# Performance work log

Hardware: AMD Instinct MI355X
Metric: run time of the kernel (lower is better)

The kernel has to match this reference:

```python
import jax, jax.numpy as jnp
import numpy as np

EMBED_DIM = 1024
NUM_HEADS = 16
HEAD_DIM = EMBED_DIM // NUM_HEADS


def setup_inputs() -> dict:
    key = jax.random.key(0)
    k_h, k_q, k_k, k_v, k_o = jax.random.split(key, 5)
    scale = 1.0 / np.sqrt(EMBED_DIM)
    return {
        "h": jax.random.normal(k_h, (2, 2048, EMBED_DIM), dtype=jnp.float32),
        "W_q": jax.random.normal(k_q, (EMBED_DIM, EMBED_DIM), dtype=jnp.float32) * scale,
        "W_k": jax.random.normal(k_k, (EMBED_DIM, EMBED_DIM), dtype=jnp.float32) * scale,
        "W_v": jax.random.normal(k_v, (EMBED_DIM, EMBED_DIM), dtype=jnp.float32) * scale,
        "W_o": jax.random.normal(k_o, (EMBED_DIM, EMBED_DIM), dtype=jnp.float32) * scale,
    }


def reference(h, W_q, W_k, W_v, W_o):
    B, S, E = h.shape
    H, D = NUM_HEADS, HEAD_DIM
    # nn.Linear stores weight as [out, in]; y = x @ W.T
    q = (h @ W_q.T).reshape(B, S, H, D).transpose(0, 2, 1, 3)  # [B,H,S,D]
    k = (h @ W_k.T).reshape(B, S, H, D).transpose(0, 2, 1, 3)
    v = (h @ W_v.T).reshape(B, S, H, D).transpose(0, 2, 1, 3)
    scores = jnp.einsum("bhsd,bhtd->bhst", q, k) / np.sqrt(D)
    attn = jax.nn.softmax(scores, axis=-1)
    ctx = jnp.einsum("bhst,bhtd->bhsd", attn, v)  # [B,H,S,D]
    ctx = ctx.transpose(0, 2, 1, 3).reshape(B, S, E)
    return ctx @ W_o.T
```

## Files before the change

kernel.cpp:

```cpp
#include <hip/hip_runtime.h>

#define B_ 2
#define S_ 2048
#define E_ 1024
#define H_ 16
#define D_ 64
#define M_ (B_*S_)

typedef __attribute__((ext_vector_type(8))) short bf16x8;
typedef __attribute__((ext_vector_type(4))) float f32x4;
typedef __attribute__((ext_vector_type(8))) unsigned short u16x8;
typedef __attribute__((ext_vector_type(4))) unsigned short u16x4;

__device__ __forceinline__ unsigned short f2bf(float f) {
  union { float f; unsigned u; } a; a.f = f;
  unsigned u = a.u;
  return (unsigned short)((u + 0x7FFFu + ((u >> 16) & 1u)) >> 16);
}

__device__ __forceinline__ void gload_lds16(const void* g, void* l) {
  __builtin_amdgcn_global_load_lds(
      (const __attribute__((address_space(1))) void*)g,
      (__attribute__((address_space(3))) void*)l, 16, 0, 0);
}

__global__ __launch_bounds__(256) void cvt_bf16(const float* __restrict__ src,
                                                unsigned short* __restrict__ dst,
                                                int n4, float scale) {
  int i = blockIdx.x * blockDim.x + threadIdx.x;
  if (i < n4) {
    float4 v = ((const float4*)src)[i];
    u16x4 o;
    o[0] = f2bf(v.x * scale);
    o[1] = f2bf(v.y * scale);
    o[2] = f2bf(v.z * scale);
    o[3] = f2bf(v.w * scale);
    ((u16x4*)dst)[i] = o;
  }
}

template<int OUT_BF16>
__device__ __forceinline__ void gemm_body(const unsigned short* __restrict__ A,
                                          const unsigned short* __restrict__ W,
                                          void* __restrict__ Cv,
                                          int row0, int col0, int N, int K,
                                          unsigned short* As, unsigned short* Bs) {
  const int tid = threadIdx.x;
  const int lane = tid & 63, wave = tid >> 6;
  const int wr = wave >> 1, wc = wave & 1;
  const int lq = lane & 15, lg = lane >> 4;
  f32x4 acc[4][4] = {};

  for (int kt = 0; kt < K; kt += 32) {
#pragma unroll
    for (int i = 0; i < 2; ++i) {
      int t = tid + i * 256;
      int rr = t >> 2;
      int sch = (t & 3) ^ ((rr >> 1) & 3);
      gload_lds16(A + (size_t)(row0 + rr) * K + kt + sch * 8, &As[t * 8]);
      gload_lds16(W + (size_t)(col0 + rr) * K + kt + sch * 8, &Bs[t * 8]);
    }
    __syncthreads();
    bf16x8 af[4], bfr[4];
#pragma unroll
    for (int mi = 0; mi < 4; ++mi) {
      int row = wr * 64 + mi * 16 + lq;
      af[mi] = *(const bf16x8*)&As[row * 32 + (lg ^ ((row >> 1) & 3)) * 8];
    }
#pragma unroll
    for (int ni = 0; ni < 4; ++ni) {
      int row = wc * 64 + ni * 16 + lq;
      bfr[ni] = *(const bf16x8*)&Bs[row * 32 + (lg ^ ((row >> 1) & 3)) * 8];
    }
#pragma unroll
    for (int mi = 0; mi < 4; ++mi)
#pragma unroll
      for (int ni = 0; ni < 4; ++ni)
        acc[mi][ni] = __builtin_amdgcn_mfma_f32_16x16x32_bf16(af[mi], bfr[ni], acc[mi][ni], 0, 0, 0);
    __syncthreads();
  }

#pragma unroll
  for (int mi = 0; mi < 4; ++mi)
#pragma unroll
    for (int ni = 0; ni < 4; ++ni) {
      int row = row0 + wr * 64 + mi * 16 + lg * 4;
      int col = col0 + wc * 64 + ni * 16 + lq;
#pragma unroll
      for (int r = 0; r < 4; ++r) {
        float v = acc[mi][ni][r];
        if (OUT_BF16) ((unsigned short*)Cv)[(size_t)(row + r) * N + col] = f2bf(v);
        else          ((float*)Cv)[(size_t)(row + r) * N + col] = v;
      }
    }
}

__global__ __launch_bounds__(256) void gemm_qkv(const unsigned short* __restrict__ A,
                                                const unsigned short* __restrict__ Wq,
                                                const unsigned short* __restrict__ Wk,
                                                const unsigned short* __restrict__ Wv,
                                                unsigned short* __restrict__ Qb,
                                                unsigned short* __restrict__ Kb,
                                                unsigned short* __restrict__ Vb) {
  __shared__ unsigned short As[128 * 32];
  __shared__ unsigned short Bs[128 * 32];
  const int mat = blockIdx.y >> 3;
  const int col0 = (blockIdx.y & 7) * 128;
  const unsigned short* W = (mat == 0) ? Wq : (mat == 1) ? Wk : Wv;
  unsigned short* C = (mat == 0) ? Qb : (mat == 1) ? Kb : Vb;
  gemm_body<1>(A, W, C, blockIdx.x * 128, col0, E_, E_, As, Bs);
}

__global__ __launch_bounds__(256) void gemm_out(const unsigned short* __restrict__ A,
                                                const unsigned short* __restrict__ W,
                                                float* __restrict__ C) {
  __shared__ unsigned short As[128 * 32];
  __shared__ unsigned short Bs[128 * 32];
  gemm_body<0>(A, W, C, blockIdx.x * 128, blockIdx.y * 128, E_, E_, As, Bs);
}

__global__ __launch_bounds__(256) void transpose_v(const unsigned short* __restrict__ V,
                                                   unsigned short* __restrict__ VT) {
  __shared__ unsigned short tile[64][72];
  const int tid = threadIdx.x;
  const int s0 = blockIdx.x * 64;
  const int h = blockIdx.y;
  const int b = blockIdx.z;
  const int r = tid >> 3;
  const int c = (tid & 7) * 8;
  const unsigned short* src = V + ((size_t)(b * S_) + s0) * E_ + h * 64;
#pragma unroll
  for (int i = 0; i < 2; ++i) {
    int rr = r + i * 32;
    u16x8 v = *(const u16x8*)(src + (size_t)rr * E_ + c);
#pragma unroll
    for (int j = 0; j < 8; ++j) tile[rr][c + j] = v[j];
  }
  __syncthreads();
  unsigned short* dst = VT + ((size_t)((b * H_ + h) * 64)) * S_ + s0;
#pragma unroll
  for (int i = 0; i < 2; ++i) {
    int d = r + i * 32;
    u16x8 o;
#pragma unroll
    for (int j = 0; j < 8; ++j) o[j] = tile[c + j][d];
    *(u16x8*)(dst + (size_t)d * S_ + c) = o;
  }
}

__global__ __launch_bounds__(256) void attn(const unsigned short* __restrict__ Q,
                                            const unsigned short* __restrict__ K,
                                            const unsigned short* __restrict__ VT,
                                            unsigned short* __restrict__ ctx) {
  __shared__ unsigned short Ks[64 * 64];
  __shared__ unsigned short Vs[64 * 64];
  __shared__ unsigned short Ps[4][16 * 72];
  const int tid = threadIdx.x, lane = tid & 63, wave = tid >> 6;
  const int lq = lane & 15, lg = lane >> 4;
  const int bh = blockIdx.y, b = bh >> 4, h = bh & 15;
  const int q0 = blockIdx.x * 64;

  const unsigned short* Qbase = Q + ((size_t)(b * S_) + q0 + wave * 16 + lq) * E_ + h * 64;
  bf16x8 qf0 = *(const bf16x8*)(Qbase + lg * 8);
  bf16x8 qf1 = *(const bf16x8*)(Qbase + 32 + lg * 8);
  const unsigned short* Kbase = K + (size_t)(b * S_) * E_ + h * 64;
  const unsigned short* Vtb = VT + (size_t)((b * H_ + h) * 64) * S_;

  f32x4 oacc[4] = {};
  float m_run = -1e30f, l_run = 0.f;

  for (int kc = 0; kc < S_; kc += 64) {
    __syncthreads();
#pragma unroll
    for (int i = 0; i < 2; ++i) {
      int tt = tid + i * 256;
      int r = tt >> 3;
      int sch = (tt & 7) ^ (r & 7);
      gload_lds16(Kbase + (size_t)(kc + r) * E_ + sch * 8, &Ks[tt * 8]);
      gload_lds16(Vtb + (size_t)r * S_ + kc + sch * 8, &Vs[tt * 8]);
    }
    __syncthreads();

    f32x4 st[4] = {};
#pragma unroll
    for (int mf = 0; mf < 4; ++mf) {
      int row = mf * 16 + lq;
      bf16x8 kf0 = *(const bf16x8*)&Ks[row * 64 + ((lg ^ (row & 7)) * 8)];
      bf16x8 kf1 = *(const bf16x8*)&Ks[row * 64 + (((4 + lg) ^ (row & 7)) * 8)];
      st[mf] = __builtin_amdgcn_mfma_f32_16x16x32_bf16(kf0, qf0, st[mf], 0, 0, 0);
      st[mf] = __builtin_amdgcn_mfma_f32_16x16x32_bf16(kf1, qf1, st[mf], 0, 0, 0);
    }

    float c0 = fmaxf(fmaxf(st[0][0], st[0][1]), fmaxf(st[0][2], st[0][3]));
    float c1 = fmaxf(fmaxf(st[1][0], st[1][1]), fmaxf(st[1][2], st[1][3]));
    float c2 = fmaxf(fmaxf(st[2][0], st[2][1]), fmaxf(st[2][2], st[2][3]));
    float c3 = fmaxf(fmaxf(st[3][0], st[3][1]), fmaxf(st[3][2], st[3][3]));
    float cm = fmaxf(fmaxf(c0, c1), fmaxf(c2, c3));
    cm = fmaxf(cm, __shfl_xor(cm, 16));
    cm = fmaxf(cm, __shfl_xor(cm, 32));

    float m_new = fmaxf(m_run, cm);
    float alpha = __builtin_amdgcn_exp2f(m_run - m_new);

    float ls = 0.f;
#pragma unroll
    for (int mf = 0; mf < 4; ++mf) {
      u16x4 pb;
#pragma unroll
      for (int r = 0; r < 4; ++r) {
        float p = __builtin_amdgcn_exp2f(st[mf][r] - m_new);
        ls += p;
        pb[r] = f2bf(p);
      }
      *(u16x4*)&Ps[wave][lq * 72 + mf * 16 + lg * 4] = pb;
    }
    ls += __shfl_xor(ls, 16);
    ls += __shfl_xor(ls, 32);
    l_run = l_run * alpha + ls;
    m_run = m_new;
    asm volatile("s_waitcnt lgkmcnt(0)" ::: "memory");

#pragma unroll
    for (int r = 0; r < 4; ++r) {
      float ar = __shfl(alpha, lg * 4 + r);
#pragma unroll
      for (int nf = 0; nf < 4; ++nf) oacc[nf][r] *= ar;
    }

#pragma unroll
    for (int ks = 0; ks < 2; ++ks) {
      bf16x8 pf = *(const bf16x8*)&Ps[wave][lq * 72 + ks * 32 + lg * 8];
#pragma unroll
      for (int nf = 0; nf < 4; ++nf) {
        int row = nf * 16 + lq;
        bf16x8 vf = *(const bf16x8*)&Vs[row * 64 + (((ks * 4 + lg) ^ (row & 7)) * 8)];
        oacc[nf] = __builtin_amdgcn_mfma_f32_16x16x32_bf16(pf, vf, oacc[nf], 0, 0, 0);
      }
    }
  }

#pragma unroll
  for (int r = 0; r < 4; ++r) {
    float lr = __shfl(l_run, lg * 4 + r);
    float inv = 1.f / lr;
#pragma unroll
    for (int nf = 0; nf < 4; ++nf) {
      ctx[((size_t)(b * S_) + q0 + wave * 16 + lg * 4 + r) * E_ + h * 64 + nf * 16 + lq] =
          f2bf(oacc[nf][r] * inv);
    }
  }
}

extern "C" void kernel_launch(void* const* d_in, const int* in_sizes, int n_in,
                              void* d_out, int out_size, void* d_ws, size_t ws_size,
                              hipStream_t stream) {
  const float* h  = (const float*)d_in[0];
  const float* Wq = (const float*)d_in[1];
  const float* Wk = (const float*)d_in[2];
  const float* Wv = (const float*)d_in[3];
  const float* Wo = (const float*)d_in[4];
  float* out = (float*)d_out;
  char* ws = (char*)d_ws;

  const size_t SZ_H = (size_t)M_ * E_ * 2;
  const size_t SZ_W = (size_t)E_ * E_ * 2;
  unsigned short* hb  = (unsigned short*)(ws);
  unsigned short* wqb = (unsigned short*)(ws + SZ_H);
  unsigned short* wkb = (unsigned short*)(ws + SZ_H + SZ_W);
  unsigned short* wvb = (unsigned short*)(ws + SZ_H + 2 * SZ_W);
  unsigned short* wob = (unsigned short*)(ws + SZ_H + 3 * SZ_W);
  unsigned short* Qb  = (unsigned short*)(ws + SZ_H + 4 * SZ_W);
  unsigned short* Kb  = (unsigned short*)(ws + 2 * SZ_H + 4 * SZ_W);
  unsigned short* Vb  = (unsigned short*)(ws + 3 * SZ_H + 4 * SZ_W);
  unsigned short* VTb = hb;
  unsigned short* Cb  = Vb;

  const float QSCALE = 0.125f * 1.44269504f;
  cvt_bf16<<<4096, 256, 0, stream>>>(h, hb, M_ * E_ / 4, 1.0f);
  cvt_bf16<<<1024, 256, 0, stream>>>(Wq, wqb, E_ * E_ / 4, QSCALE);
  cvt_bf16<<<1024, 256, 0, stream>>>(Wk, wkb, E_ * E_ / 4, 1.0f);
  cvt_bf16<<<1024, 256, 0, stream>>>(Wv, wvb, E_ * E_ / 4, 1.0f);
  cvt_bf16<<<1024, 256, 0, stream>>>(Wo, wob, E_ * E_ / 4, 1.0f);

  gemm_qkv<<<dim3(M_ / 128, 3 * E_ / 128), 256, 0, stream>>>(hb, wqb, wkb, wvb, Qb, Kb, Vb);

  transpose_v<<<dim3(S_ / 64, H_, B_), 256, 0, stream>>>(Vb, VTb);

  attn<<<dim3(S_ / 64, B_ * H_), 256, 0, stream>>>(Qb, Kb, VTb, Cb);

  gemm_out<<<dim3(M_ / 128, E_ / 128), 256, 0, stream>>>(Cb, wob, out);
}
```

Measured before the change: 225.2 us.

## Double-buffer attention K/V tiles, lazy softmax rescale, fuse bf16 conversions

The attention kernel now prefetches the next K/V tile into a second LDS buffer while the current one is computed, so the load-then-barrier stall at the top of each iteration goes away. The online softmax skips the running-max update and output rescale unless the new max exceeds the old one by more than 8 (log2 units), which cuts exp and multiply work per tile. The five fp32-to-bf16 conversion launches are merged into one kernel. The manual rounding routine is replaced with the library __float2bfloat16 conversion. The extra buffers double the K/V LDS footprint, and the lazy rescale lets unnormalised probabilities grow up to 2^8 before they are converted to bf16.

After: 225.6 us. No clear change (+0.2%).

```diff
diff --git a/kernel.cpp b/kernel.cpp
--- a/kernel.cpp
+++ b/kernel.cpp
@@ -1,4 +1,5 @@
 #include <hip/hip_runtime.h>
+#include <hip/hip_bf16.h>
 
 #define B_ 2
 #define S_ 2048
@@ -12,10 +13,10 @@
 typedef __attribute__((ext_vector_type(8))) unsigned short u16x8;
 typedef __attribute__((ext_vector_type(4))) unsigned short u16x4;
 
-__device__ __forceinline__ unsigned short f2bf(float f) {
-  union { float f; unsigned u; } a; a.f = f;
-  unsigned u = a.u;
-  return (unsigned short)((u + 0x7FFFu + ((u >> 16) & 1u)) >> 16);
+__device__ __forceinline__ unsigned short f2bf_hw(float f) {
+  union { __hip_bfloat16 h; unsigned short u; } c;
+  c.h = __float2bfloat16(f);
+  return c.u;
 }
 
 __device__ __forceinline__ void gload_lds16(const void* g, void* l) {
@@ -24,19 +25,33 @@
       (__attribute__((address_space(3))) void*)l, 16, 0, 0);
 }
 
-__global__ __launch_bounds__(256) void cvt_bf16(const float* __restrict__ src,
-                                                unsigned short* __restrict__ dst,
-                                                int n4, float scale) {
-  int i = blockIdx.x * blockDim.x + threadIdx.x;
-  if (i < n4) {
-    float4 v = ((const float4*)src)[i];
-    u16x4 o;
-    o[0] = f2bf(v.x * scale);
-    o[1] = f2bf(v.y * scale);
-    o[2] = f2bf(v.z * scale);
-    o[3] = f2bf(v.w * scale);
-    ((u16x4*)dst)[i] = o;
-  }
+__global__ __launch_bounds__(256) void cvt_all(const float* __restrict__ h,
+                                               const float* __restrict__ Wq,
+                                               const float* __restrict__ Wk,
+                                               const float* __restrict__ Wv,
+                                               const float* __restrict__ Wo,
+                                               unsigned short* __restrict__ dst,
+                                               float qscale) {
+  int i = blockIdx.x * 256 + threadIdx.x;
+  const float4* src4;
+  int idx;
+  float scale = 1.f;
+  if (i < (1 << 20)) {
+    src4 = (const float4*)h; idx = i;
+  } else {
+    int t = i - (1 << 20);
+    int j = t >> 18;
+    idx = t & ((1 << 18) - 1);
+    src4 = (const float4*)((j == 0) ? Wq : (j == 1) ? Wk : (j == 2) ? Wv : Wo);
+    if (j == 0) scale = qscale;
+  }
+  float4 v = src4[idx];
+  u16x4 o;
+  o[0] = f2bf_hw(v.x * scale);
+  o[1] = f2bf_hw(v.y * scale);
+  o[2] = f2bf_hw(v.z * scale);
+  o[3] = f2bf_hw(v.w * scale);
+  ((u16x4*)dst)[i] = o;
 }
 
 template<int OUT_BF16>
@@ -89,7 +104,7 @@
 #pragma unroll
       for (int r = 0; r < 4; ++r) {
         float v = acc[mi][ni][r];
-        if (OUT_BF16) ((unsigned short*)Cv)[(size_t)(row + r) * N + col] = f2bf(v);
+        if (OUT_BF16) ((unsigned short*)Cv)[(size_t)(row + r) * N + col] = f2bf_hw(v);
         else          ((float*)Cv)[(size_t)(row + r) * N + col] = v;
       }
     }
@@ -152,8 +167,8 @@
                                             const unsigned short* __restrict__ K,
                                             const unsigned short* __restrict__ VT,
                                             unsigned short* __restrict__ ctx) {
-  __shared__ unsigned short Ks[64 * 64];
-  __shared__ unsigned short Vs[64 * 64];
+  __shared__ unsigned short Ks[2][64 * 64];
+  __shared__ unsigned short Vs[2][64 * 64];
   __shared__ unsigned short Ps[4][16 * 72];
   const int tid = threadIdx.x, lane = tid & 63, wave = tid >> 6;
   const int lq = lane & 15, lg = lane >> 4;
@@ -165,28 +180,40 @@
   bf16x8 qf1 = *(const bf16x8*)(Qbase + 32 + lg * 8);
   const unsigned short* Kbase = K + (size_t)(b * S_) * E_ + h * 64;
   const unsigned short* Vtb = VT + (size_t)((b * H_ + h) * 64) * S_;
-
-  f32x4 oacc[4] = {};
-  float m_run = -1e30f, l_run = 0.f;
-
-  for (int kc = 0; kc < S_; kc += 64) {
-    __syncthreads();
+  unsigned short* Pw = Ps[wave];
+
+  auto STAGE = [&](int buf, int kc) {
 #pragma unroll
     for (int i = 0; i < 2; ++i) {
       int tt = tid + i * 256;
       int r = tt >> 3;
       int sch = (tt & 7) ^ (r & 7);
-      gload_lds16(Kbase + (size_t)(kc + r) * E_ + sch * 8, &Ks[tt * 8]);
-      gload_lds16(Vtb + (size_t)r * S_ + kc + sch * 8, &Vs[tt * 8]);
-    }
-    __syncthreads();
+      gload_lds16(Kbase + (size_t)(kc + r) * E_ + sch * 8, &Ks[buf][tt * 8]);
+      gload_lds16(Vtb + (size_t)r * S_ + kc + sch * 8, &Vs[buf][tt * 8]);
+    }
+  };
+
+  f32x4 oacc[4] = {};
+  float m_run = -1e30f, l_run = 0.f;
+
+  STAGE(0, 0);
+  asm volatile("s_waitcnt vmcnt(0)" ::: "memory");
+  __builtin_amdgcn_s_barrier();
+
+  int cur = 0;
+  for (int kc = 0; kc < S_; kc += 64) {
+    const bool pref = (kc + 64 < S_);
+    if (pref) STAGE(cur ^ 1, kc + 64);
+
+    const unsigned short* Kc = Ks[cur];
+    const unsigned short* Vc = Vs[cur];
 
     f32x4 st[4] = {};
 #pragma unroll
     for (int mf = 0; mf < 4; ++mf) {
       int row = mf * 16 + lq;
-      bf16x8 kf0 = *(const bf16x8*)&Ks[row * 64 + ((lg ^ (row & 7)) * 8)];
-      bf16x8 kf1 = *(const bf16x8*)&Ks[row * 64 + (((4 + lg) ^ (row & 7)) * 8)];
+      bf16x8 kf0 = *(const bf16x8*)&Kc[row * 64 + ((lg ^ (row & 7)) * 8)];
+      bf16x8 kf1 = *(const bf16x8*)&Kc[row * 64 + (((4 + lg) ^ (row & 7)) * 8)];
       st[mf] = __builtin_amdgcn_mfma_f32_16x16x32_bf16(kf0, qf0, st[mf], 0, 0, 0);
       st[mf] = __builtin_amdgcn_mfma_f32_16x16x32_bf16(kf1, qf1, st[mf], 0, 0, 0);
     }
@@ -199,8 +226,18 @@
     cm = fmaxf(cm, __shfl_xor(cm, 16));
     cm = fmaxf(cm, __shfl_xor(cm, 32));
 
-    float m_new = fmaxf(m_run, cm);
-    float alpha = __builtin_amdgcn_exp2f(m_run - m_new);
+    if (!__all(cm - m_run <= 8.f)) {
+      float m_new = fmaxf(m_run, cm);
+      float alpha = __builtin_amdgcn_exp2f(m_run - m_new);
+#pragma unroll
+      for (int r = 0; r < 4; ++r) {
+        float ar = __shfl(alpha, lg * 4 + r);
+#pragma unroll
+        for (int nf = 0; nf < 4; ++nf) oacc[nf][r] *= ar;
+      }
+      l_run *= alpha;
+      m_run = m_new;
+    }
 
     float ls = 0.f;
 #pragma unroll
@@ -208,34 +245,32 @@
       u16x4 pb;
 #pragma unroll
       for (int r = 0; r < 4; ++r) {
-        float p = __builtin_amdgcn_exp2f(st[mf][r] - m_new);
+        float p = __builtin_amdgcn_exp2f(st[mf][r] - m_run);
         ls += p;
-        pb[r] = f2bf(p);
+        pb[r] = f2bf_hw(p);
       }
-      *(u16x4*)&Ps[wave][lq * 72 + mf * 16 + lg * 4] = pb;
+      *(u16x4*)&Pw[lq * 72 + mf * 16 + lg * 4] = pb;
     }
     ls += __shfl_xor(ls, 16);
     ls += __shfl_xor(ls, 32);
-    l_run = l_run * alpha + ls;
-    m_run = m_new;
+    l_run += ls;
     asm volatile("s_waitcnt lgkmcnt(0)" ::: "memory");
 
 #pragma unroll
-    for (int r = 0; r < 4; ++r) {
-      float ar = __shfl(alpha, lg * 4 + r);
-#pragma unroll
-      for (int nf = 0; nf < 4; ++nf) oacc[nf][r] *= ar;
-    }
-
-#pragma unroll
     for (int ks = 0; ks < 2; ++ks) {
-      bf16x8 pf = *(const bf16x8*)&Ps[wave][lq * 72 + ks * 32 + lg * 8];
+      bf16x8 pf = *(const bf16x8*)&Pw[lq * 72 + ks * 32 + lg * 8];
 #pragma unroll
       for (int nf = 0; nf < 4; ++nf) {
         int row = nf * 16 + lq;
-        bf16x8 vf = *(const bf16x8*)&Vs[row * 64 + (((ks * 4 + lg) ^ (row & 7)) * 8)];
+        bf16x8 vf = *(const bf16x8*)&Vc[row * 64 + (((ks * 4 + lg) ^ (row & 7)) * 8)];
         oacc[nf] = __builtin_amdgcn_mfma_f32_16x16x32_bf16(pf, vf, oacc[nf], 0, 0, 0);
       }
+    }
+
+    if (pref) {
+      asm volatile("s_waitcnt vmcnt(0)" ::: "memory");
+      __builtin_amdgcn_s_barrier();
+      cur ^= 1;
     }
   }
 
@@ -246,7 +281,7 @@
 #pragma unroll
     for (int nf = 0; nf < 4; ++nf) {
       ctx[((size_t)(b * S_) + q0 + wave * 16 + lg * 4 + r) * E_ + h * 64 + nf * 16 + lq] =
-          f2bf(oacc[nf][r] * inv);
+          f2bf_hw(oacc[nf][r] * inv);
     }
   }
 }
@@ -276,11 +311,7 @@
   unsigned short* Cb  = Vb;
 
   const float QSCALE = 0.125f * 1.44269504f;
-  cvt_bf16<<<4096, 256, 0, stream>>>(h, hb, M_ * E_ / 4, 1.0f);
-  cvt_bf16<<<1024, 256, 0, stream>>>(Wq, wqb, E_ * E_ / 4, QSCALE);
-  cvt_bf16<<<1024, 256, 0, stream>>>(Wk, wkb, E_ * E_ / 4, 1.0f);
-  cvt_bf16<<<1024, 256, 0, stream>>>(Wv, wvb, E_ * E_ / 4, 1.0f);
-  cvt_bf16<<<1024, 256, 0, stream>>>(Wo, wob, E_ * E_ / 4, 1.0f);
+  cvt_all<<<8192, 256, 0, stream>>>(h, Wq, Wk, Wv, Wo, hb, QSCALE);
 
   gemm_qkv<<<dim3(M_ / 128, 3 * E_ / 128), 256, 0, stream>>>(hb, wqb, wkb, wvb, Qb, Kb, Vb);
 
```
